# Performance work log

Measured on AMD Instinct MI355X. Metric: run time of the kernel, lower is better.

Reference implementation:

```python
import jax, jax.numpy as jnp
import numpy as np

B = 16      # number of point clouds
N = 16384   # points per cloud
K = 4096    # nb_vertices sampled per cloud (ratio = 0.25)


def _fps_single(pts, k):
    """Deterministic farthest-point sampling on one cloud.
    pts: [N, 3]. Start from index 0 (deterministic start), then iteratively
    pick the point with max min-distance to the selected set.
    Returns int32 indices [k].
    """
    mind0 = jnp.sum((pts - pts[0]) ** 2, axis=-1)  # [N] squared dists to seed

    def step(mind, _):
        idx = jnp.argmax(mind)                                   # farthest point
        d = jnp.sum((pts - pts[idx]) ** 2, axis=-1)              # [N]
        return jnp.minimum(mind, d), idx.astype(jnp.int32)

    _, idxs = jax.lax.scan(step, mind0, None, length=k - 1)
    return jnp.concatenate([jnp.zeros((1,), jnp.int32), idxs])


def setup_inputs() -> dict:
    key = jax.random.key(0)
    x = jax.random.normal(key, (B * N, 3), dtype=jnp.float32)
    batch = jnp.repeat(jnp.arange(B, dtype=jnp.int32), N)  # sorted cloud ids
    return {"x": x, "batch": batch}


def reference(x, batch):
    # ratio = K / N != 1, so the module runs fps and gathers.
    pts = x.reshape(B, N, 3)
    idxs = jax.vmap(lambda p: _fps_single(p, K))(pts)                 # [B, K]
    sampled = jnp.take_along_axis(pts, idxs[:, :, None], axis=1)      # [B, K, 3]
    x_out = sampled.reshape(B * K, 3)
    batch_out = jnp.repeat(jnp.arange(B, dtype=batch.dtype), K)       # [B*K]
    return (x_out, batch_out)
```

## Files before the change

kernel.cpp:

```cpp
#include <hip/hip_runtime.h>
#include <cstdint>

#pragma clang fp contract(off)

#define B_ 16
#define N_ 16384
#define K_ 4096
#define THREADS_ 1024
#define PTS_ (N_ / THREADS_)
#define NW_ (THREADS_ / 64)

#define PTS_LIST(X) \
  X(0) X(1) X(2) X(3) X(4) X(5) X(6) X(7) \
  X(8) X(9) X(10) X(11) X(12) X(13) X(14) X(15)

__device__ __forceinline__ float bfr(float f) {
  union { float f; uint32_t i; } c; c.f = f;
  c.i = (c.i + 0x7FFFu + ((c.i >> 16) & 1u)) & 0xFFFF0000u;
  return c.f;
}

template <int CTRL>
__device__ __forceinline__ float dpp_fmax(float v) {
  union { float f; int i; } s, p;
  s.f = v;
  p.i = __builtin_amdgcn_update_dpp(0, s.i, CTRL, 0xF, 0xF, false);
  return fmaxf(v, p.f);
}
template <int CTRL>
__device__ __forceinline__ unsigned dpp_umin(unsigned v) {
  const int p = __builtin_amdgcn_update_dpp((int)0xFFFFFFFFu, (int)v,
                                            CTRL, 0xF, 0xF, false);
  const unsigned pu = (unsigned)p;
  return pu < v ? pu : v;
}

__device__ __forceinline__ void wave_argmax(float bv, unsigned bg,
                                            float& wv, unsigned& wg) {
  float v = bv;
  v = dpp_fmax<0x111>(v);
  v = dpp_fmax<0x112>(v);
  v = dpp_fmax<0x114>(v);
  v = dpp_fmax<0x118>(v);
  v = dpp_fmax<0x142>(v);
  v = dpp_fmax<0x143>(v);
  union { float f; int i; } mx;
  mx.i = __builtin_amdgcn_readlane(__builtin_bit_cast(int, v), 63);
  unsigned c = (bv == mx.f) ? bg : 0xFFFFFFFFu;
  c = dpp_umin<0x111>(c);
  c = dpp_umin<0x112>(c);
  c = dpp_umin<0x114>(c);
  c = dpp_umin<0x118>(c);
  c = dpp_umin<0x142>(c);
  c = dpp_umin<0x143>(c);
  wg = (unsigned)__builtin_amdgcn_readlane((int)c, 63);
  wv = mx.f;
}

template <int CTRL>
__device__ __forceinline__ unsigned long long kmax_dpp(unsigned long long k) {
  const int lo = (int)(unsigned)k;
  const int hi = (int)(unsigned)(k >> 32);
  const int plo = __builtin_amdgcn_update_dpp(lo, lo, CTRL, 0xF, 0xF, true);
  const int phi = __builtin_amdgcn_update_dpp(hi, hi, CTRL, 0xF, 0xF, true);
  const unsigned long long ok =
      ((unsigned long long)(unsigned)phi << 32) | (unsigned)plo;
  return ok > k ? ok : k;
}

__global__ __attribute__((amdgpu_flat_work_group_size(THREADS_, THREADS_),
                          amdgpu_waves_per_eu(4, 4)))
void fps_kernel(const float* __restrict__ x, float* __restrict__ out)
{
#pragma clang fp contract(off)
  const int b    = blockIdx.x;
  const int t    = threadIdx.x;
  const int lane = t & 63;
  const int wave = t >> 6;

  __shared__ float2 s_xy[N_];
  __shared__ unsigned long long s_key[2][NW_];

  const float* xb  = x + (size_t)b * (N_ * 3);
  float* out_x     = out;
  float* out_batch = out + (size_t)B_ * K_ * 3;

  {
    const float bb = (float)b;
    for (int i = t; i < K_; i += THREADS_) out_batch[b * K_ + i] = bb;
  }

#define DECLP(i) float pz##i, m##i;
  PTS_LIST(DECLP)
#undef DECLP

#define LOADP(i) { const float* p_ = xb + 3 * ((i) * THREADS_ + t); \
                   float2 v_; v_.x = p_[0]; v_.y = p_[1];           \
                   s_xy[(i) * THREADS_ + t] = v_;                   \
                   pz##i = p_[2]; m##i = __builtin_inff(); }
  PTS_LIST(LOADP)
#undef LOADP

#define UPD(i) { const float2 v_ = s_xy[(i) * THREADS_ + t];                    \
                 const float dx_ = v_.x - cx;                                   \
                 const float dy_ = v_.y - cy;                                   \
                 const float dz_ = pz##i - cz;                                  \
                 const float d_  = __builtin_fmaf(dz_, dz_,                     \
                                   __builtin_fmaf(dx_, dx_, dy_ * dy_));        \
                 m##i = fminf(m##i, d_); }

#define MAXTREE(M_) { const float t0_ = fmaxf(fmaxf(m0,  m1),  m2);  \
                      const float t1_ = fmaxf(fmaxf(m3,  m4),  m5);  \
                      const float t2_ = fmaxf(fmaxf(m6,  m7),  m8);  \
                      const float t3_ = fmaxf(fmaxf(m9,  m10), m11); \
                      const float t4_ = fmaxf(fmaxf(m12, m13), m14); \
                      const float u0_ = fmaxf(fmaxf(t0_, t1_), t2_); \
                      const float u1_ = fmaxf(fmaxf(t3_, t4_), m15); \
                      M_ = fmaxf(u0_, u1_); }

#define IDXCHAIN(M_, BS_) { BS_ = 15;                                \
      if (m14 == M_) BS_ = 14; if (m13 == M_) BS_ = 13;              \
      if (m12 == M_) BS_ = 12; if (m11 == M_) BS_ = 11;              \
      if (m10 == M_) BS_ = 10; if (m9  == M_) BS_ = 9;               \
      if (m8  == M_) BS_ = 8;  if (m7  == M_) BS_ = 7;               \
      if (m6  == M_) BS_ = 6;  if (m5  == M_) BS_ = 5;               \
      if (m4  == M_) BS_ = 4;  if (m3  == M_) BS_ = 3;               \
      if (m2  == M_) BS_ = 2;  if (m1  == M_) BS_ = 1;               \
      if (m0  == M_) BS_ = 0; }

#define REDUCE_AND_POST(PARITY) {                                        \
      float bv; int bs;                                                  \
      MAXTREE(bv)                                                        \
      IDXCHAIN(bv, bs)                                                   \
      const unsigned bg = (unsigned)(bs * THREADS_ + t);                 \
      float wv; unsigned wg;                                             \
      wave_argmax(bv, bg, wv, wg);                                       \
      if (lane == 0) {                                                   \
        union { float f; unsigned u; } cv; cv.f = wv;                    \
        s_key[PARITY][wave] =                                            \
            ((unsigned long long)cv.u << 32) | (unsigned)~wg;            \
      } }

  float cx = xb[0], cy = xb[1], cz = xb[2];
  if (t == 0) {
    const uint64_t o = ((uint64_t)b * K_) * 3;
    out_x[o + 0] = bfr(cx); out_x[o + 1] = bfr(cy); out_x[o + 2] = bfr(cz);
  }

  PTS_LIST(UPD)
  REDUCE_AND_POST(0)
  __syncthreads();

  for (int j = 1; j < K_; ++j) {
    const int rp = (j - 1) & 1;
    const int wp = j & 1;

    unsigned long long k = s_key[rp][lane & 15];
    k = kmax_dpp<0xB1>(k);
    k = kmax_dpp<0x4E>(k);
    k = kmax_dpp<0x141>(k);
    k = kmax_dpp<0x140>(k);
    const unsigned idx = ~(unsigned)k;
    const int gu = __builtin_amdgcn_readfirstlane((int)idx);

    const float2 cxy = s_xy[gu];
    cx = cxy.x; cy = cxy.y;
    cz = xb[3 * gu + 2];
    if (t == 0) {
      const uint64_t o = ((uint64_t)b * K_ + j) * 3;
      out_x[o + 0] = bfr(cx); out_x[o + 1] = bfr(cy); out_x[o + 2] = bfr(cz);
    }

    PTS_LIST(UPD)
    REDUCE_AND_POST(wp)
    __syncthreads();
  }
#undef UPD
#undef MAXTREE
#undef IDXCHAIN
#undef REDUCE_AND_POST

}

extern "C" void kernel_launch(void* const* d_in, const int* in_sizes, int n_in,
                              void* d_out, int out_size, void* d_ws, size_t ws_size,
                              hipStream_t stream) {
  const float* x = (const float*)d_in[0];
  float* out     = (float*)d_out;
  (void)in_sizes; (void)n_in; (void)out_size; (void)d_ws; (void)ws_size;
  hipLaunchKernelGGL(fps_kernel, dim3(B_), dim3(THREADS_), 0, stream, x, out);
}
```

Baseline: 5.470 ms.

## Pack point pairs into float2 vectors and restructure LDS into padded SoA

Result: slower. 6.289 ms (+15.0%).

```diff
diff --git a/kernel.cpp b/kernel.cpp
--- a/kernel.cpp
+++ b/kernel.cpp
@@ -9,10 +9,11 @@
 #define THREADS_ 1024
 #define PTS_ (N_ / THREADS_)
 #define NW_ (THREADS_ / 64)
-
-#define PTS_LIST(X) \
-  X(0) X(1) X(2) X(3) X(4) X(5) X(6) X(7) \
-  X(8) X(9) X(10) X(11) X(12) X(13) X(14) X(15)
+#define STRIDE_ 17
+
+typedef float f2 __attribute__((ext_vector_type(2)));
+
+#define PAIR_LIST(X) X(0) X(1) X(2) X(3) X(4) X(5) X(6) X(7)
 
 __device__ __forceinline__ float bfr(float f) {
   union { float f; uint32_t i; } c; c.f = f;
@@ -78,7 +79,8 @@
   const int lane = t & 63;
   const int wave = t >> 6;
 
-  __shared__ float2 s_xy[N_];
+  __shared__ float s_x[THREADS_ * STRIDE_];
+  __shared__ float s_y[THREADS_ * STRIDE_];
   __shared__ unsigned long long s_key[2][NW_];
 
   const float* xb  = x + (size_t)b * (N_ * 3);
@@ -90,43 +92,50 @@
     for (int i = t; i < K_; i += THREADS_) out_batch[b * K_ + i] = bb;
   }
 
-#define DECLP(i) float pz##i, m##i;
-  PTS_LIST(DECLP)
+#define DECLP(p) f2 pz##p, pm##p;
+  PAIR_LIST(DECLP)
 #undef DECLP
 
-#define LOADP(i) { const float* p_ = xb + 3 * ((i) * THREADS_ + t); \
-                   float2 v_; v_.x = p_[0]; v_.y = p_[1];           \
-                   s_xy[(i) * THREADS_ + t] = v_;                   \
-                   pz##i = p_[2]; m##i = __builtin_inff(); }
-  PTS_LIST(LOADP)
+#define LOADP(p) { const float* a_ = xb + 3 * ((2*(p)) * THREADS_ + t);      \
+                   const float* b2_ = xb + 3 * ((2*(p)+1) * THREADS_ + t);   \
+                   s_x[t * STRIDE_ + 2*(p)]     = a_[0];                     \
+                   s_x[t * STRIDE_ + 2*(p) + 1] = b2_[0];                    \
+                   s_y[t * STRIDE_ + 2*(p)]     = a_[1];                     \
+                   s_y[t * STRIDE_ + 2*(p) + 1] = b2_[1];                    \
+                   pz##p.x = a_[2]; pz##p.y = b2_[2];                        \
+                   pm##p.x = __builtin_inff(); pm##p.y = __builtin_inff(); }
+  PAIR_LIST(LOADP)
 #undef LOADP
 
-#define UPD(i) { const float2 v_ = s_xy[(i) * THREADS_ + t];                    \
-                 const float dx_ = v_.x - cx;                                   \
-                 const float dy_ = v_.y - cy;                                   \
-                 const float dz_ = pz##i - cz;                                  \
-                 const float d_  = __builtin_fmaf(dz_, dz_,                     \
-                                   __builtin_fmaf(dx_, dx_, dy_ * dy_));        \
-                 m##i = fminf(m##i, d_); }
-
-#define MAXTREE(M_) { const float t0_ = fmaxf(fmaxf(m0,  m1),  m2);  \
-                      const float t1_ = fmaxf(fmaxf(m3,  m4),  m5);  \
-                      const float t2_ = fmaxf(fmaxf(m6,  m7),  m8);  \
-                      const float t3_ = fmaxf(fmaxf(m9,  m10), m11); \
-                      const float t4_ = fmaxf(fmaxf(m12, m13), m14); \
-                      const float u0_ = fmaxf(fmaxf(t0_, t1_), t2_); \
-                      const float u1_ = fmaxf(fmaxf(t3_, t4_), m15); \
+#define UPD(p) { const int a_ = t * STRIDE_ + 2*(p);                          \
+                 f2 vx_; vx_.x = s_x[a_]; vx_.y = s_x[a_ + 1];                \
+                 f2 vy_; vy_.x = s_y[a_]; vy_.y = s_y[a_ + 1];                \
+                 const f2 dx_ = vx_ - cx2;                                    \
+                 const f2 dy_ = vy_ - cy2;                                    \
+                 const f2 dz_ = pz##p - cz2;                                  \
+                 const f2 d_  = __builtin_elementwise_fma(dz_, dz_,           \
+                                __builtin_elementwise_fma(dx_, dx_,           \
+                                                          dy_ * dy_));        \
+                 pm##p = __builtin_elementwise_min(pm##p, d_); }
+
+#define MAXTREE(M_) { const float t0_ = fmaxf(fmaxf(pm0.x, pm0.y), pm1.x);   \
+                      const float t1_ = fmaxf(fmaxf(pm1.y, pm2.x), pm2.y);   \
+                      const float t2_ = fmaxf(fmaxf(pm3.x, pm3.y), pm4.x);   \
+                      const float t3_ = fmaxf(fmaxf(pm4.y, pm5.x), pm5.y);   \
+                      const float t4_ = fmaxf(fmaxf(pm6.x, pm6.y), pm7.x);   \
+                      const float u0_ = fmaxf(fmaxf(t0_, t1_), t2_);         \
+                      const float u1_ = fmaxf(fmaxf(t3_, t4_), pm7.y);       \
                       M_ = fmaxf(u0_, u1_); }
 
-#define IDXCHAIN(M_, BS_) { BS_ = 15;                                \
-      if (m14 == M_) BS_ = 14; if (m13 == M_) BS_ = 13;              \
-      if (m12 == M_) BS_ = 12; if (m11 == M_) BS_ = 11;              \
-      if (m10 == M_) BS_ = 10; if (m9  == M_) BS_ = 9;               \
-      if (m8  == M_) BS_ = 8;  if (m7  == M_) BS_ = 7;               \
-      if (m6  == M_) BS_ = 6;  if (m5  == M_) BS_ = 5;               \
-      if (m4  == M_) BS_ = 4;  if (m3  == M_) BS_ = 3;               \
-      if (m2  == M_) BS_ = 2;  if (m1  == M_) BS_ = 1;               \
-      if (m0  == M_) BS_ = 0; }
+#define IDXCHAIN(M_, BS_) { BS_ = 15;                                        \
+      if (pm7.x == M_) BS_ = 14; if (pm6.y == M_) BS_ = 13;                  \
+      if (pm6.x == M_) BS_ = 12; if (pm5.y == M_) BS_ = 11;                  \
+      if (pm5.x == M_) BS_ = 10; if (pm4.y == M_) BS_ = 9;                   \
+      if (pm4.x == M_) BS_ = 8;  if (pm3.y == M_) BS_ = 7;                   \
+      if (pm3.x == M_) BS_ = 6;  if (pm2.y == M_) BS_ = 5;                   \
+      if (pm2.x == M_) BS_ = 4;  if (pm1.y == M_) BS_ = 3;                   \
+      if (pm1.x == M_) BS_ = 2;  if (pm0.y == M_) BS_ = 1;                   \
+      if (pm0.x == M_) BS_ = 0; }
 
 #define REDUCE_AND_POST(PARITY) {                                        \
       float bv; int bs;                                                  \
@@ -147,8 +156,13 @@
     out_x[o + 0] = bfr(cx); out_x[o + 1] = bfr(cy); out_x[o + 2] = bfr(cz);
   }
 
-  PTS_LIST(UPD)
-  REDUCE_AND_POST(0)
+  {
+    f2 cx2; cx2.x = cx; cx2.y = cx;
+    f2 cy2; cy2.x = cy; cy2.y = cy;
+    f2 cz2; cz2.x = cz; cz2.y = cz;
+    PAIR_LIST(UPD)
+    REDUCE_AND_POST(0)
+  }
   __syncthreads();
 
   for (int j = 1; j < K_; ++j) {
@@ -163,16 +177,23 @@
     const unsigned idx = ~(unsigned)k;
     const int gu = __builtin_amdgcn_readfirstlane((int)idx);
 
-    const float2 cxy = s_xy[gu];
-    cx = cxy.x; cy = cxy.y;
+    const int tg = gu & (THREADS_ - 1);
+    const int ig = gu >> 10;
+    cx = s_x[tg * STRIDE_ + ig];
+    cy = s_y[tg * STRIDE_ + ig];
     cz = xb[3 * gu + 2];
     if (t == 0) {
       const uint64_t o = ((uint64_t)b * K_ + j) * 3;
       out_x[o + 0] = bfr(cx); out_x[o + 1] = bfr(cy); out_x[o + 2] = bfr(cz);
     }
 
-    PTS_LIST(UPD)
-    REDUCE_AND_POST(wp)
+    {
+      f2 cx2; cx2.x = cx; cx2.y = cx;
+      f2 cy2; cy2.x = cy; cy2.y = cy;
+      f2 cz2; cz2.x = cz; cz2.y = cz;
+      PAIR_LIST(UPD)
+      REDUCE_AND_POST(wp)
+    }
     __syncthreads();
   }
 #undef UPD
```

## Keep point coordinates in registers and publish winner coordinates per wave

Applied to the files above, without the earlier changes.

Result: slower. 8.542 ms (+56.2%).

```diff
diff --git a/kernel.cpp b/kernel.cpp
--- a/kernel.cpp
+++ b/kernel.cpp
@@ -7,7 +7,6 @@
 #define N_ 16384
 #define K_ 4096
 #define THREADS_ 1024
-#define PTS_ (N_ / THREADS_)
 #define NW_ (THREADS_ / 64)
 
 #define PTS_LIST(X) \
@@ -68,6 +67,8 @@
   return ok > k ? ok : k;
 }
 
+struct alignas(16) Cand { float cx, cy, cz, pad; };
+
 __global__ __attribute__((amdgpu_flat_work_group_size(THREADS_, THREADS_),
                           amdgpu_waves_per_eu(4, 4)))
 void fps_kernel(const float* __restrict__ x, float* __restrict__ out)
@@ -78,8 +79,8 @@
   const int lane = t & 63;
   const int wave = t >> 6;
 
-  __shared__ float2 s_xy[N_];
-  __shared__ unsigned long long s_key[2][NW_];
+  __shared__ unsigned long long s_key[2][3200];
+  __shared__ Cand               s_cand[2][2176];
 
   const float* xb  = x + (size_t)b * (N_ * 3);
   float* out_x     = out;
@@ -90,20 +91,18 @@
     for (int i = t; i < K_; i += THREADS_) out_batch[b * K_ + i] = bb;
   }
 
-#define DECLP(i) float pz##i, m##i;
+#define DECLP(i) float px##i, py##i, pz##i, m##i;
   PTS_LIST(DECLP)
 #undef DECLP
 
 #define LOADP(i) { const float* p_ = xb + 3 * ((i) * THREADS_ + t); \
-                   float2 v_; v_.x = p_[0]; v_.y = p_[1];           \
-                   s_xy[(i) * THREADS_ + t] = v_;                   \
-                   pz##i = p_[2]; m##i = __builtin_inff(); }
+                   px##i = p_[0]; py##i = p_[1]; pz##i = p_[2];     \
+                   m##i = __builtin_inff(); }
   PTS_LIST(LOADP)
 #undef LOADP
 
-#define UPD(i) { const float2 v_ = s_xy[(i) * THREADS_ + t];                    \
-                 const float dx_ = v_.x - cx;                                   \
-                 const float dy_ = v_.y - cy;                                   \
+#define UPD(i) { const float dx_ = px##i - cx;                                  \
+                 const float dy_ = py##i - cy;                                  \
                  const float dz_ = pz##i - cz;                                  \
                  const float d_  = __builtin_fmaf(dz_, dz_,                     \
                                    __builtin_fmaf(dx_, dx_, dy_ * dy_));        \
@@ -128,17 +127,45 @@
       if (m2  == M_) BS_ = 2;  if (m1  == M_) BS_ = 1;               \
       if (m0  == M_) BS_ = 0; }
 
-#define REDUCE_AND_POST(PARITY) {                                        \
+#define REDUCE_AND_POST(P) {                                             \
       float bv; int bs;                                                  \
       MAXTREE(bv)                                                        \
       IDXCHAIN(bv, bs)                                                   \
       const unsigned bg = (unsigned)(bs * THREADS_ + t);                 \
       float wv; unsigned wg;                                             \
       wave_argmax(bv, bg, wv, wg);                                       \
+      const unsigned wgu = (unsigned)__builtin_amdgcn_readfirstlane((int)wg); \
+      const unsigned su  = wgu >> 10;                                    \
+      float sx = px0, sy = py0, sz = pz0;                                \
+      if (su == 1)  { sx = px1;  sy = py1;  sz = pz1;  }                 \
+      if (su == 2)  { sx = px2;  sy = py2;  sz = pz2;  }                 \
+      if (su == 3)  { sx = px3;  sy = py3;  sz = pz3;  }                 \
+      if (su == 4)  { sx = px4;  sy = py4;  sz = pz4;  }                 \
+      if (su == 5)  { sx = px5;  sy = py5;  sz = pz5;  }                 \
+      if (su == 6)  { sx = px6;  sy = py6;  sz = pz6;  }                 \
+      if (su == 7)  { sx = px7;  sy = py7;  sz = pz7;  }                 \
+      if (su == 8)  { sx = px8;  sy = py8;  sz = pz8;  }                 \
+      if (su == 9)  { sx = px9;  sy = py9;  sz = pz9;  }                 \
+      if (su == 10) { sx = px10; sy = py10; sz = pz10; }                 \
+      if (su == 11) { sx = px11; sy = py11; sz = pz11; }                 \
+      if (su == 12) { sx = px12; sy = py12; sz = pz12; }                 \
+      if (su == 13) { sx = px13; sy = py13; sz = pz13; }                 \
+      if (su == 14) { sx = px14; sy = py14; sz = pz14; }                 \
+      if (su == 15) { sx = px15; sy = py15; sz = pz15; }                 \
+      const int ol_ = (int)(wgu & 63u);                                  \
+      const int cxi = __builtin_amdgcn_readlane(__builtin_bit_cast(int, sx), ol_); \
+      const int cyi = __builtin_amdgcn_readlane(__builtin_bit_cast(int, sy), ol_); \
+      const int czi = __builtin_amdgcn_readlane(__builtin_bit_cast(int, sz), ol_); \
       if (lane == 0) {                                                   \
         union { float f; unsigned u; } cv; cv.f = wv;                    \
-        s_key[PARITY][wave] =                                            \
-            ((unsigned long long)cv.u << 32) | (unsigned)~wg;            \
+        s_key[P][wave] =                                                 \
+            ((unsigned long long)cv.u << 32) | (unsigned)~wgu;           \
+        Cand c_;                                                         \
+        c_.cx = __builtin_bit_cast(float, cxi);                          \
+        c_.cy = __builtin_bit_cast(float, cyi);                          \
+        c_.cz = __builtin_bit_cast(float, czi);                          \
+        c_.pad = 0.0f;                                                   \
+        s_cand[P][wave] = c_;                                            \
       } }
 
   float cx = xb[0], cy = xb[1], cz = xb[2];
@@ -156,16 +183,20 @@
     const int wp = j & 1;
 
     unsigned long long k = s_key[rp][lane & 15];
+    const Cand cd = s_cand[rp][lane & 15];
     k = kmax_dpp<0xB1>(k);
     k = kmax_dpp<0x4E>(k);
     k = kmax_dpp<0x141>(k);
     k = kmax_dpp<0x140>(k);
-    const unsigned idx = ~(unsigned)k;
-    const int gu = __builtin_amdgcn_readfirstlane((int)idx);
-
-    const float2 cxy = s_xy[gu];
-    cx = cxy.x; cy = cxy.y;
-    cz = xb[3 * gu + 2];
+    const unsigned g = ~(unsigned)k;
+    const int gu = __builtin_amdgcn_readfirstlane((int)g);
+    const int ws = (gu >> 6) & 15;
+    cx = __builtin_bit_cast(float,
+           __builtin_amdgcn_readlane(__builtin_bit_cast(int, cd.cx), ws));
+    cy = __builtin_bit_cast(float,
+           __builtin_amdgcn_readlane(__builtin_bit_cast(int, cd.cy), ws));
+    cz = __builtin_bit_cast(float,
+           __builtin_amdgcn_readlane(__builtin_bit_cast(int, cd.cz), ws));
     if (t == 0) {
       const uint64_t o = ((uint64_t)b * K_ + j) * 3;
       out_x[o + 0] = bfr(cx); out_x[o + 1] = bfr(cy); out_x[o + 2] = bfr(cz);
```

## Split each cloud across two workgroups with global-memory argmax handshake

Applied to the files above, without the earlier changes.

Measured after the change: 21.47 ms. +292.4%, slower.

```diff
diff --git a/kernel.cpp b/kernel.cpp
--- a/kernel.cpp
+++ b/kernel.cpp
@@ -6,13 +6,13 @@
 #define B_ 16
 #define N_ 16384
 #define K_ 4096
+#define G_ 2
 #define THREADS_ 1024
-#define PTS_ (N_ / THREADS_)
+#define PPB_ (N_ / G_)
 #define NW_ (THREADS_ / 64)
-
-#define PTS_LIST(X) \
-  X(0) X(1) X(2) X(3) X(4) X(5) X(6) X(7) \
-  X(8) X(9) X(10) X(11) X(12) X(13) X(14) X(15)
+#define XYPAD_ 11264
+
+#define PTS_LIST(X) X(0) X(1) X(2) X(3) X(4) X(5) X(6) X(7)
 
 __device__ __forceinline__ float bfr(float f) {
   union { float f; uint32_t i; } c; c.f = f;
@@ -70,15 +70,19 @@
 
 __global__ __attribute__((amdgpu_flat_work_group_size(THREADS_, THREADS_),
                           amdgpu_waves_per_eu(4, 4)))
-void fps_kernel(const float* __restrict__ x, float* __restrict__ out)
+void fps_kernel(const float* __restrict__ x, float* __restrict__ out,
+                unsigned long long* __restrict__ wkeys,
+                unsigned* __restrict__ wtags)
 {
 #pragma clang fp contract(off)
-  const int b    = blockIdx.x;
+  const int bid  = blockIdx.x;
+  const int b    = bid & 15;
+  const int r    = bid >> 4;
   const int t    = threadIdx.x;
   const int lane = t & 63;
   const int wave = t >> 6;
 
-  __shared__ float2 s_xy[N_];
+  __shared__ float2 s_xy[XYPAD_];
   __shared__ unsigned long long s_key[2][NW_];
 
   const float* xb  = x + (size_t)b * (N_ * 3);
@@ -94,9 +98,9 @@
   PTS_LIST(DECLP)
 #undef DECLP
 
-#define LOADP(i) { const float* p_ = xb + 3 * ((i) * THREADS_ + t); \
-                   float2 v_; v_.x = p_[0]; v_.y = p_[1];           \
-                   s_xy[(i) * THREADS_ + t] = v_;                   \
+#define LOADP(i) { const float* p_ = xb + 3 * (r * PPB_ + (i) * THREADS_ + t); \
+                   float2 v_; v_.x = p_[0]; v_.y = p_[1];                      \
+                   s_xy[(i) * THREADS_ + t] = v_;                              \
                    pz##i = p_[2]; m##i = __builtin_inff(); }
   PTS_LIST(LOADP)
 #undef LOADP
@@ -109,30 +113,21 @@
                                    __builtin_fmaf(dx_, dx_, dy_ * dy_));        \
                  m##i = fminf(m##i, d_); }
 
-#define MAXTREE(M_) { const float t0_ = fmaxf(fmaxf(m0,  m1),  m2);  \
-                      const float t1_ = fmaxf(fmaxf(m3,  m4),  m5);  \
-                      const float t2_ = fmaxf(fmaxf(m6,  m7),  m8);  \
-                      const float t3_ = fmaxf(fmaxf(m9,  m10), m11); \
-                      const float t4_ = fmaxf(fmaxf(m12, m13), m14); \
-                      const float u0_ = fmaxf(fmaxf(t0_, t1_), t2_); \
-                      const float u1_ = fmaxf(fmaxf(t3_, t4_), m15); \
-                      M_ = fmaxf(u0_, u1_); }
-
-#define IDXCHAIN(M_, BS_) { BS_ = 15;                                \
-      if (m14 == M_) BS_ = 14; if (m13 == M_) BS_ = 13;              \
-      if (m12 == M_) BS_ = 12; if (m11 == M_) BS_ = 11;              \
-      if (m10 == M_) BS_ = 10; if (m9  == M_) BS_ = 9;               \
-      if (m8  == M_) BS_ = 8;  if (m7  == M_) BS_ = 7;               \
-      if (m6  == M_) BS_ = 6;  if (m5  == M_) BS_ = 5;               \
-      if (m4  == M_) BS_ = 4;  if (m3  == M_) BS_ = 3;               \
-      if (m2  == M_) BS_ = 2;  if (m1  == M_) BS_ = 1;               \
-      if (m0  == M_) BS_ = 0; }
+#define MAXTREE(M_) { const float t0_ = fmaxf(fmaxf(m0, m1), m2);    \
+                      const float t1_ = fmaxf(fmaxf(m3, m4), m5);    \
+                      M_ = fmaxf(fmaxf(t0_, t1_), fmaxf(m6, m7)); }
+
+#define IDXCHAIN(M_, BS_) { BS_ = 7;                                 \
+      if (m6 == M_) BS_ = 6; if (m5 == M_) BS_ = 5;                  \
+      if (m4 == M_) BS_ = 4; if (m3 == M_) BS_ = 3;                  \
+      if (m2 == M_) BS_ = 2; if (m1 == M_) BS_ = 1;                  \
+      if (m0 == M_) BS_ = 0; }
 
 #define REDUCE_AND_POST(PARITY) {                                        \
       float bv; int bs;                                                  \
       MAXTREE(bv)                                                        \
       IDXCHAIN(bv, bs)                                                   \
-      const unsigned bg = (unsigned)(bs * THREADS_ + t);                 \
+      const unsigned bg = (unsigned)(r * PPB_ + bs * THREADS_ + t);      \
       float wv; unsigned wg;                                             \
       wave_argmax(bv, bg, wv, wg);                                       \
       if (lane == 0) {                                                   \
@@ -142,7 +137,7 @@
       } }
 
   float cx = xb[0], cy = xb[1], cz = xb[2];
-  if (t == 0) {
+  if (r == 0 && t == 0) {
     const uint64_t o = ((uint64_t)b * K_) * 3;
     out_x[o + 0] = bfr(cx); out_x[o + 1] = bfr(cy); out_x[o + 2] = bfr(cz);
   }
@@ -154,19 +149,41 @@
   for (int j = 1; j < K_; ++j) {
     const int rp = (j - 1) & 1;
     const int wp = j & 1;
-
-    unsigned long long k = s_key[rp][lane & 15];
-    k = kmax_dpp<0xB1>(k);
-    k = kmax_dpp<0x4E>(k);
-    k = kmax_dpp<0x141>(k);
-    k = kmax_dpp<0x140>(k);
-    const unsigned idx = ~(unsigned)k;
+    const int gp = j & 1;
+
+    unsigned long long bk = s_key[rp][lane & 15];
+    bk = kmax_dpp<0xB1>(bk);
+    bk = kmax_dpp<0x4E>(bk);
+    bk = kmax_dpp<0x141>(bk);
+    bk = kmax_dpp<0x140>(bk);
+
+    const int widx = ((b << 1) | gp) * G_ + r;
+    const int ridx = ((b << 1) | gp) * G_ + (1 - r);
+    if (t == 0) {
+      __hip_atomic_store(&wkeys[widx], bk, __ATOMIC_RELAXED,
+                         __HIP_MEMORY_SCOPE_AGENT);
+      __hip_atomic_store(&wtags[widx], (unsigned)j, __ATOMIC_RELEASE,
+                         __HIP_MEMORY_SCOPE_AGENT);
+    }
+
+    unsigned tg;
+    do {
+      tg = __hip_atomic_load(&wtags[ridx], __ATOMIC_RELAXED,
+                             __HIP_MEMORY_SCOPE_AGENT);
+    } while (tg != (unsigned)j);
+    __builtin_amdgcn_fence(__ATOMIC_ACQUIRE, "agent");
+    const unsigned long long rk =
+        __hip_atomic_load(&wkeys[ridx], __ATOMIC_RELAXED,
+                          __HIP_MEMORY_SCOPE_AGENT);
+
+    const unsigned long long ck = rk > bk ? rk : bk;
+    const unsigned idx = ~(unsigned)ck;
     const int gu = __builtin_amdgcn_readfirstlane((int)idx);
 
-    const float2 cxy = s_xy[gu];
-    cx = cxy.x; cy = cxy.y;
+    cx = xb[3 * gu + 0];
+    cy = xb[3 * gu + 1];
     cz = xb[3 * gu + 2];
-    if (t == 0) {
+    if (r == 0 && t == 0) {
       const uint64_t o = ((uint64_t)b * K_ + j) * 3;
       out_x[o + 0] = bfr(cx); out_x[o + 1] = bfr(cy); out_x[o + 2] = bfr(cz);
     }
@@ -187,6 +204,15 @@
                               hipStream_t stream) {
   const float* x = (const float*)d_in[0];
   float* out     = (float*)d_out;
-  (void)in_sizes; (void)n_in; (void)out_size; (void)d_ws; (void)ws_size;
-  hipLaunchKernelGGL(fps_kernel, dim3(B_), dim3(THREADS_), 0, stream, x, out);
-}
+  (void)in_sizes; (void)n_in; (void)out_size; (void)ws_size;
+
+  unsigned long long* wkeys = (unsigned long long*)d_ws;
+  unsigned* wtags = (unsigned*)((char*)d_ws +
+                    (size_t)B_ * 2 * G_ * sizeof(unsigned long long));
+  const size_t sync_bytes = (size_t)B_ * 2 * G_ *
+      (sizeof(unsigned long long) + sizeof(unsigned));
+
+  hipMemsetAsync(d_ws, 0, sync_bytes, stream);
+  hipLaunchKernelGGL(fps_kernel, dim3(B_ * G_), dim3(THREADS_), 0, stream,
+                     x, out, wkeys, wtags);
+}
```
